# Performance work log

Measured on AMD Instinct MI355X. Metric: run time of the kernel, lower is better.

The kernel has to match this reference:

```python
import jax, jax.numpy as jnp
import numpy as np


def setup_inputs() -> dict:
    key = jax.random.key(0)
    kq, kk, kv = jax.random.split(key, 3)
    B, HQ, HKV, S, D = 1, 32, 8, 2048, 128
    return {
        "query": jax.random.normal(kq, (B, HQ, S, D), dtype=jnp.float32),
        "key": jax.random.normal(kk, (B, HKV, S, D), dtype=jnp.float32),
        "value": jax.random.normal(kv, (B, HKV, S, D), dtype=jnp.float32),
    }


def reference(query, key, value):
    # RawSDP.forward with is_causal=True, attn_mask=None, dropout_p=0, scale=None
    b, hq, sq, d = query.shape
    hkv = key.shape[1]
    reps = hq // hkv  # GQA group size
    # repeak_kv: expand each kv head `reps` times contiguously along head axis
    key = jnp.repeat(key, reps, axis=1)    # [b, hq, skv, d]
    value = jnp.repeat(value, reps, axis=1)
    skv = key.shape[2]
    half_sqrt = 1.0 / jnp.sqrt(jnp.sqrt(jnp.float32(d)))  # scale split across q and k
    scores = jnp.einsum("bhqd,bhkd->bhqk", query * half_sqrt, key * half_sqrt)
    # causal tril bool mask -> additive mask (0 where allowed, finfo.min where not)
    causal = jnp.tril(jnp.ones((sq, skv), dtype=bool))
    neg = jnp.finfo(query.dtype).min
    scores = scores + jnp.where(causal, jnp.zeros((), query.dtype), neg)
    # softmax computed in float32, cast back to query dtype
    attn = jax.nn.softmax(scores.astype(jnp.float32), axis=-1).astype(query.dtype)
    return jnp.einsum("bhqk,bhkd->bhqd", attn, value)
```

## Files before the change

kernel.cpp:

```cpp
#include <hip/hip_runtime.h>
#include <hip/hip_bf16.h>
#include <stdint.h>

typedef __attribute__((ext_vector_type(8))) short bf16x8;
typedef __attribute__((ext_vector_type(4))) float f32x4;
typedef __attribute__((ext_vector_type(16))) float f32x16;

#define S_LEN 2048
#define D_DIM 128
#define HQ_N  32
#define NT32  64
#define SUB_B 8192

__device__ __forceinline__ ushort f2bf(float f) {
  union { float f; uint32_t u; } c; c.f = f;
  uint32_t u = c.u;
  u += 0x7FFFu + ((u >> 16) & 1u);
  return (ushort)(u >> 16);
}

__device__ __forceinline__ uint32_t cvtpk(float lo, float hi) {
  uint32_t r;
  asm("v_cvt_pk_bf16_f32 %0, %1, %2" : "=v"(r) : "v"(lo), "v"(hi));
  return r;
}

__device__ __forceinline__ float xhalf_max(float x) {
  uint32_t a = __builtin_bit_cast(uint32_t, x), b;
  asm volatile("v_mov_b32 %0, %1" : "=&v"(b) : "v"(a));
  asm volatile("v_permlane32_swap_b32 %0, %1" : "+v"(a), "+v"(b));
  return fmaxf(__builtin_bit_cast(float, a), __builtin_bit_cast(float, b));
}

__global__ __launch_bounds__(256) void prep_k(const float* __restrict__ K,
                                              ushort* __restrict__ KT) {
  int tid  = blockIdx.x * 256 + threadIdx.x;
  int tile = tid >> 9;
  int c    = tid & 511;
  int s    = c >> 6;
  int lane = c & 63;
  int l31  = lane & 31, hi = lane >> 5;
  const float* src = K + ((size_t)(tile * 32 + l31)) * D_DIM + 16 * s + 8 * hi;
  float4 x = *(const float4*)src;
  float4 y = *(const float4*)(src + 4);
  union { ushort u[8]; bf16x8 v; } o;
  o.u[0] = f2bf(x.x); o.u[1] = f2bf(x.y); o.u[2] = f2bf(x.z); o.u[3] = f2bf(x.w);
  o.u[4] = f2bf(y.x); o.u[5] = f2bf(y.y); o.u[6] = f2bf(y.z); o.u[7] = f2bf(y.w);
  *(bf16x8*)(KT + (size_t)tid * 8) = o.v;
}

__global__ __launch_bounds__(256) void prep_v(const float* __restrict__ V,
                                              ushort* __restrict__ VT) {
  int tid  = blockIdx.x * 256 + threadIdx.x;
  int tile = tid >> 9;
  int cc   = tid & 511;
  int l31  = cc & 31;
  int hi   = (cc >> 5) & 1;
  int c    = (cc >> 6) & 1;
  int dt   = cc >> 7;
  int hkv  = tile >> 6, ktv = tile & 63;
  const float* src = V + ((size_t)hkv * S_LEN + ktv * 32 + 16 * c + 8 * hi) * D_DIM
                       + 32 * dt + l31;
  union { ushort u[8]; bf16x8 v; } o;
  #pragma unroll
  for (int jj = 0; jj < 8; ++jj) o.u[jj] = f2bf(src[(size_t)jj * D_DIM]);
  *(bf16x8*)(VT + (size_t)tid * 8) = o.v;
}

__global__ __launch_bounds__(256, 2) void attn_fwd(
    const float* __restrict__ Q, const ushort* __restrict__ KT,
    const ushort* __restrict__ VT, float* __restrict__ O) {
  const int id   = blockIdx.x;
  const int g    = id & 7;
  const int c    = (id >> 3) & 31;
  const int p    = (id >> 8) & 1;
  const int j    = p ? (63 - c) : c;
  const int qh   = threadIdx.x >> 6;
  const int h    = g * 4 + qh;
  const int lane = threadIdx.x & 63;
  const int l31  = lane & 31;
  const int hi   = lane >> 5;
  const int qrow = j * 32 + l31;
  const int jt   = j >> 1;

  const char* kt_base = (const char*)KT + (size_t)g * NT32 * SUB_B;
  const char* vt_base = (const char*)VT + (size_t)g * NT32 * SUB_B;

  const float scale = 0.08838834764831845f * 1.4426950408889634f;
  bf16x8 qf[8];
  {
    const float* qp = Q + ((size_t)h * S_LEN + qrow) * D_DIM;
    #pragma unroll
    for (int s = 0; s < 8; ++s) {
      const float* px = qp + 16 * s + 8 * hi;
      float4 x = *(const float4*)px;
      float4 y = *(const float4*)(px + 4);
      bf16x8 f;
      f[0] = (short)f2bf(x.x * scale); f[1] = (short)f2bf(x.y * scale);
      f[2] = (short)f2bf(x.z * scale); f[3] = (short)f2bf(x.w * scale);
      f[4] = (short)f2bf(y.x * scale); f[5] = (short)f2bf(y.y * scale);
      f[6] = (short)f2bf(y.z * scale); f[7] = (short)f2bf(y.w * scale);
      qf[s] = f;
    }
  }

  bf16x8 ones;
  #pragma unroll
  for (int s = 0; s < 8; ++s) ones[s] = (short)0x3F80;
  const f32x16 zero16 = {};

  f32x16 o4[4] = {};
  float mrow = -1e30f, lsum = 0.f;

  for (int kt = 0; kt <= jt; ++kt) {
    const char* kp = kt_base + (size_t)kt * (2 * SUB_B);

    bf16x8 kf[16];
    #pragma unroll
    for (int t = 0; t < 2; ++t)
      #pragma unroll
      for (int s = 0; s < 8; ++s)
        kf[t * 8 + s] = *(const bf16x8*)(kp + t * SUB_B + (s * 64 + lane) * 16);
    bf16x8 vfA[8], vfB[8];
    const char* vp = vt_base + (size_t)(2 * kt) * SUB_B;
    #pragma unroll
    for (int ks = 0; ks < 2; ++ks)
      #pragma unroll
      for (int dt = 0; dt < 4; ++dt)
        vfA[ks * 4 + dt] = *(const bf16x8*)(vp + (dt * 128 + ks * 64 + lane) * 16);

    f32x16 st[2] = {};
    __builtin_amdgcn_s_setprio(1);
    #pragma unroll
    for (int t = 0; t < 2; ++t)
      #pragma unroll
      for (int s = 0; s < 8; ++s)
        st[t] = __builtin_amdgcn_mfma_f32_32x32x16_bf16(kf[t * 8 + s], qf[s], st[t], 0, 0, 0);
    __builtin_amdgcn_s_setprio(0);

    #pragma unroll
    for (int ks = 0; ks < 2; ++ks)
      #pragma unroll
      for (int dt = 0; dt < 4; ++dt)
        vfB[ks * 4 + dt] = *(const bf16x8*)(vp + SUB_B + (dt * 128 + ks * 64 + lane) * 16);

    if (kt == jt) {
      #pragma unroll
      for (int t = 0; t < 2; ++t)
        #pragma unroll
        for (int r = 0; r < 16; ++r) {
          int kv = 64 * kt + 32 * t + (r & 3) + 8 * (r >> 2) + 4 * hi;
          if (kv > qrow) st[t][r] = -1e30f;
        }
    }

    float t16[8];
    #pragma unroll
    for (int e = 0; e < 8; ++e)
      t16[e] = fmaxf(fmaxf(st[0][e], st[0][e + 8]), fmaxf(st[1][e], st[1][e + 8]));
    float mx = fmaxf(fmaxf(fmaxf(t16[0], t16[1]), fmaxf(t16[2], t16[3])),
                     fmaxf(fmaxf(t16[4], t16[5]), fmaxf(t16[6], t16[7])));
    mx = xhalf_max(mx);
    if (!__all(mx <= mrow + 8.0f)) {
      float mnew = fmaxf(mrow, mx);
      float alpha = exp2f(mrow - mnew);
      #pragma unroll
      for (int dt = 0; dt < 4; ++dt) o4[dt] *= alpha;
      lsum *= alpha;
      mrow = mnew;
    }
    #pragma unroll
    for (int t = 0; t < 2; ++t)
      #pragma unroll
      for (int e = 0; e < 16; ++e) st[t][e] = exp2f(st[t][e] - mrow);

    bf16x8 pb[4];
    #pragma unroll
    for (int t = 0; t < 2; ++t)
      #pragma unroll
      for (int cc = 0; cc < 2; ++cc) {
        const int r0 = cc * 8;
        uint32_t a0 = cvtpk(st[t][r0 + 0], st[t][r0 + 1]);
        uint32_t b0 = cvtpk(st[t][r0 + 4], st[t][r0 + 5]);
        asm volatile("v_permlane32_swap_b32 %0, %1" : "+v"(a0), "+v"(b0));
        uint32_t a1 = cvtpk(st[t][r0 + 2], st[t][r0 + 3]);
        uint32_t b1 = cvtpk(st[t][r0 + 6], st[t][r0 + 7]);
        asm volatile("v_permlane32_swap_b32 %0, %1" : "+v"(a1), "+v"(b1));
        union { uint32_t u[4]; bf16x8 v; } pu;
        pu.u[0] = a0; pu.u[1] = a1; pu.u[2] = b0; pu.u[3] = b1;
        pb[t * 2 + cc] = pu.v;
      }

    f32x16 pbsum = __builtin_amdgcn_mfma_f32_32x32x16_bf16(ones, pb[0], zero16, 0, 0, 0);
    pbsum = __builtin_amdgcn_mfma_f32_32x32x16_bf16(ones, pb[1], pbsum, 0, 0, 0);
    pbsum = __builtin_amdgcn_mfma_f32_32x32x16_bf16(ones, pb[2], pbsum, 0, 0, 0);
    pbsum = __builtin_amdgcn_mfma_f32_32x32x16_bf16(ones, pb[3], pbsum, 0, 0, 0);

    __builtin_amdgcn_s_setprio(1);
    #pragma unroll
    for (int dt = 0; dt < 4; ++dt) {
      o4[dt] = __builtin_amdgcn_mfma_f32_32x32x16_bf16(vfA[0 * 4 + dt], pb[0], o4[dt], 0, 0, 0);
      o4[dt] = __builtin_amdgcn_mfma_f32_32x32x16_bf16(vfA[1 * 4 + dt], pb[1], o4[dt], 0, 0, 0);
      o4[dt] = __builtin_amdgcn_mfma_f32_32x32x16_bf16(vfB[0 * 4 + dt], pb[2], o4[dt], 0, 0, 0);
      o4[dt] = __builtin_amdgcn_mfma_f32_32x32x16_bf16(vfB[1 * 4 + dt], pb[3], o4[dt], 0, 0, 0);
    }
    __builtin_amdgcn_s_setprio(0);

    lsum += pbsum[0];

    __syncthreads();
  }

  const float inv = 1.0f / lsum;
  float* op = O + ((size_t)h * S_LEN + qrow) * D_DIM;
  #pragma unroll
  for (int dt = 0; dt < 4; ++dt)
    #pragma unroll
    for (int rq = 0; rq < 4; ++rq) {
      f32x4 vv;
      #pragma unroll
      for (int jj = 0; jj < 4; ++jj) vv[jj] = o4[dt][rq * 4 + jj] * inv;
      *(f32x4*)(op + 32 * dt + 8 * rq + 4 * hi) = vv;
    }
}

extern "C" void kernel_launch(void* const* d_in, const int* in_sizes, int n_in,
                              void* d_out, int out_size, void* d_ws, size_t ws_size,
                              hipStream_t stream) {
  const float* Q = (const float*)d_in[0];
  const float* K = (const float*)d_in[1];
  const float* V = (const float*)d_in[2];
  float* O = (float*)d_out;
  ushort* wsK = (ushort*)d_ws;
  ushort* wsV = wsK + (size_t)8 * NT32 * (SUB_B / 2);
  prep_k<<<1024, 256, 0, stream>>>(K, wsK);
  prep_v<<<1024, 256, 0, stream>>>(V, wsV);
  attn_fwd<<<512, 256, 0, stream>>>(Q, wsK, wsV, O);
}
```

Baseline: 84.88 us.

## Share K/V tiles across waves via double-buffered LDS with async global-to-LDS loads

```diff
diff --git a/kernel.cpp b/kernel.cpp
--- a/kernel.cpp
+++ b/kernel.cpp
@@ -11,6 +11,7 @@
 #define HQ_N  32
 #define NT32  64
 #define SUB_B 8192
+#define TILE_B 16384
 
 __device__ __forceinline__ ushort f2bf(float f) {
   union { float f; uint32_t u; } c; c.f = f;
@@ -30,6 +31,12 @@
   asm volatile("v_mov_b32 %0, %1" : "=&v"(b) : "v"(a));
   asm volatile("v_permlane32_swap_b32 %0, %1" : "+v"(a), "+v"(b));
   return fmaxf(__builtin_bit_cast(float, a), __builtin_bit_cast(float, b));
+}
+
+__device__ __forceinline__ void gload16(const void* g, void* l) {
+  __builtin_amdgcn_global_load_lds(
+      (const __attribute__((address_space(1))) uint32_t*)g,
+      (__attribute__((address_space(3))) uint32_t*)l, 16, 0, 0);
 }
 
 __global__ __launch_bounds__(256) void prep_k(const float* __restrict__ K,
@@ -74,17 +81,29 @@
   const int g    = id & 7;
   const int c    = (id >> 3) & 31;
   const int p    = (id >> 8) & 1;
-  const int j    = p ? (63 - c) : c;
-  const int qh   = threadIdx.x >> 6;
-  const int h    = g * 4 + qh;
+  const int qt   = p ? (15 - (c >> 2)) : (c >> 2);
+  const int h    = g * 4 + (c & 3);
+  const int w    = threadIdx.x >> 6;
   const int lane = threadIdx.x & 63;
   const int l31  = lane & 31;
   const int hi   = lane >> 5;
-  const int qrow = j * 32 + l31;
-  const int jt   = j >> 1;
+  const int qw   = qt * 128 + w * 32;
+  const int qrow = qw + l31;
+  const int ntiles = 2 * qt + 2;
+
+  __shared__ ushort Klds[2][TILE_B / 2];
+  __shared__ ushort Vlds[2][TILE_B / 2];
 
   const char* kt_base = (const char*)KT + (size_t)g * NT32 * SUB_B;
   const char* vt_base = (const char*)VT + (size_t)g * NT32 * SUB_B;
+  const int tid = threadIdx.x;
+
+  #pragma unroll
+  for (int i = 0; i < 4; ++i) {
+    int off = (tid + i * 256) * 16;
+    gload16(kt_base + off, (char*)Klds[0] + off);
+    gload16(vt_base + off, (char*)Vlds[0] + off);
+  }
 
   const float scale = 0.08838834764831845f * 1.4426950408889634f;
   bf16x8 qf[8];
@@ -112,102 +131,118 @@
   f32x16 o4[4] = {};
   float mrow = -1e30f, lsum = 0.f;
 
-  for (int kt = 0; kt <= jt; ++kt) {
-    const char* kp = kt_base + (size_t)kt * (2 * SUB_B);
-
-    bf16x8 kf[16];
-    #pragma unroll
-    for (int t = 0; t < 2; ++t)
-      #pragma unroll
-      for (int s = 0; s < 8; ++s)
-        kf[t * 8 + s] = *(const bf16x8*)(kp + t * SUB_B + (s * 64 + lane) * 16);
-    bf16x8 vfA[8], vfB[8];
-    const char* vp = vt_base + (size_t)(2 * kt) * SUB_B;
-    #pragma unroll
-    for (int ks = 0; ks < 2; ++ks)
-      #pragma unroll
-      for (int dt = 0; dt < 4; ++dt)
-        vfA[ks * 4 + dt] = *(const bf16x8*)(vp + (dt * 128 + ks * 64 + lane) * 16);
-
-    f32x16 st[2] = {};
-    __builtin_amdgcn_s_setprio(1);
-    #pragma unroll
-    for (int t = 0; t < 2; ++t)
-      #pragma unroll
-      for (int s = 0; s < 8; ++s)
-        st[t] = __builtin_amdgcn_mfma_f32_32x32x16_bf16(kf[t * 8 + s], qf[s], st[t], 0, 0, 0);
-    __builtin_amdgcn_s_setprio(0);
-
-    #pragma unroll
-    for (int ks = 0; ks < 2; ++ks)
-      #pragma unroll
-      for (int dt = 0; dt < 4; ++dt)
-        vfB[ks * 4 + dt] = *(const bf16x8*)(vp + SUB_B + (dt * 128 + ks * 64 + lane) * 16);
-
-    if (kt == jt) {
-      #pragma unroll
-      for (int t = 0; t < 2; ++t)
-        #pragma unroll
-        for (int r = 0; r < 16; ++r) {
-          int kv = 64 * kt + 32 * t + (r & 3) + 8 * (r >> 2) + 4 * hi;
-          if (kv > qrow) st[t][r] = -1e30f;
+  __syncthreads();
+
+  for (int kt = 0; kt < ntiles; ++kt) {
+    const int cur = kt & 1;
+
+    if (kt + 1 < ntiles) {
+      const char* gk = kt_base + (size_t)(kt + 1) * TILE_B;
+      const char* gv = vt_base + (size_t)(kt + 1) * TILE_B;
+      #pragma unroll
+      for (int i = 0; i < 4; ++i) {
+        int off = (tid + i * 256) * 16;
+        gload16(gk + off, (char*)Klds[cur ^ 1] + off);
+        gload16(gv + off, (char*)Vlds[cur ^ 1] + off);
+      }
+    }
+
+    if (64 * kt <= qw + 31) {
+      const char* kp = (const char*)Klds[cur];
+      const char* vp = (const char*)Vlds[cur];
+
+      bf16x8 kf[16];
+      #pragma unroll
+      for (int t = 0; t < 2; ++t)
+        #pragma unroll
+        for (int s = 0; s < 8; ++s)
+          kf[t * 8 + s] = *(const bf16x8*)(kp + t * SUB_B + (s * 64 + lane) * 16);
+      bf16x8 vfA[8], vfB[8];
+      #pragma unroll
+      for (int ks = 0; ks < 2; ++ks)
+        #pragma unroll
+        for (int dt = 0; dt < 4; ++dt)
+          vfA[ks * 4 + dt] = *(const bf16x8*)(vp + (dt * 128 + ks * 64 + lane) * 16);
+
+      f32x16 st[2] = {};
+      __builtin_amdgcn_s_setprio(1);
+      #pragma unroll
+      for (int t = 0; t < 2; ++t)
+        #pragma unroll
+        for (int s = 0; s < 8; ++s)
+          st[t] = __builtin_amdgcn_mfma_f32_32x32x16_bf16(kf[t * 8 + s], qf[s], st[t], 0, 0, 0);
+      __builtin_amdgcn_s_setprio(0);
+
+      #pragma unroll
+      for (int ks = 0; ks < 2; ++ks)
+        #pragma unroll
+        for (int dt = 0; dt < 4; ++dt)
+          vfB[ks * 4 + dt] = *(const bf16x8*)(vp + SUB_B + (dt * 128 + ks * 64 + lane) * 16);
+
+      if (64 * kt + 63 > qw) {
+        #pragma unroll
+        for (int t = 0; t < 2; ++t)
+          #pragma unroll
+          for (int r = 0; r < 16; ++r) {
+            int kv = 64 * kt + 32 * t + (r & 3) + 8 * (r >> 2) + 4 * hi;
+            if (kv > qrow) st[t][r] = -1e30f;
+          }
+      }
+
+      float t16[8];
+      #pragma unroll
+      for (int e = 0; e < 8; ++e)
+        t16[e] = fmaxf(fmaxf(st[0][e], st[0][e + 8]), fmaxf(st[1][e], st[1][e + 8]));
+      float mx = fmaxf(fmaxf(fmaxf(t16[0], t16[1]), fmaxf(t16[2], t16[3])),
+                       fmaxf(fmaxf(t16[4], t16[5]), fmaxf(t16[6], t16[7])));
+      mx = xhalf_max(mx);
+      if (!__all(mx <= mrow + 8.0f)) {
+        float mnew = fmaxf(mrow, mx);
+        float alpha = exp2f(mrow - mnew);
+        #pragma unroll
+        for (int dt = 0; dt < 4; ++dt) o4[dt] *= alpha;
+        lsum *= alpha;
+        mrow = mnew;
+      }
+      #pragma unroll
+      for (int t = 0; t < 2; ++t)
+        #pragma unroll
+        for (int e = 0; e < 16; ++e) st[t][e] = exp2f(st[t][e] - mrow);
+
+      bf16x8 pb[4];
+      #pragma unroll
+      for (int t = 0; t < 2; ++t)
+        #pragma unroll
+        for (int cc = 0; cc < 2; ++cc) {
+          const int r0 = cc * 8;
+          uint32_t a0 = cvtpk(st[t][r0 + 0], st[t][r0 + 1]);
+          uint32_t b0 = cvtpk(st[t][r0 + 4], st[t][r0 + 5]);
+          asm volatile("v_permlane32_swap_b32 %0, %1" : "+v"(a0), "+v"(b0));
+          uint32_t a1 = cvtpk(st[t][r0 + 2], st[t][r0 + 3]);
+          uint32_t b1 = cvtpk(st[t][r0 + 6], st[t][r0 + 7]);
+          asm volatile("v_permlane32_swap_b32 %0, %1" : "+v"(a1), "+v"(b1));
+          union { uint32_t u[4]; bf16x8 v; } pu;
+          pu.u[0] = a0; pu.u[1] = a1; pu.u[2] = b0; pu.u[3] = b1;
+          pb[t * 2 + cc] = pu.v;
         }
-    }
-
-    float t16[8];
-    #pragma unroll
-    for (int e = 0; e < 8; ++e)
-      t16[e] = fmaxf(fmaxf(st[0][e], st[0][e + 8]), fmaxf(st[1][e], st[1][e + 8]));
-    float mx = fmaxf(fmaxf(fmaxf(t16[0], t16[1]), fmaxf(t16[2], t16[3])),
-                     fmaxf(fmaxf(t16[4], t16[5]), fmaxf(t16[6], t16[7])));
-    mx = xhalf_max(mx);
-    if (!__all(mx <= mrow + 8.0f)) {
-      float mnew = fmaxf(mrow, mx);
-      float alpha = exp2f(mrow - mnew);
-      #pragma unroll
-      for (int dt = 0; dt < 4; ++dt) o4[dt] *= alpha;
-      lsum *= alpha;
-      mrow = mnew;
-    }
-    #pragma unroll
-    for (int t = 0; t < 2; ++t)
-      #pragma unroll
-      for (int e = 0; e < 16; ++e) st[t][e] = exp2f(st[t][e] - mrow);
-
-    bf16x8 pb[4];
-    #pragma unroll
-    for (int t = 0; t < 2; ++t)
-      #pragma unroll
-      for (int cc = 0; cc < 2; ++cc) {
-        const int r0 = cc * 8;
-        uint32_t a0 = cvtpk(st[t][r0 + 0], st[t][r0 + 1]);
-        uint32_t b0 = cvtpk(st[t][r0 + 4], st[t][r0 + 5]);
-        asm volatile("v_permlane32_swap_b32 %0, %1" : "+v"(a0), "+v"(b0));
-        uint32_t a1 = cvtpk(st[t][r0 + 2], st[t][r0 + 3]);
-        uint32_t b1 = cvtpk(st[t][r0 + 6], st[t][r0 + 7]);
-        asm volatile("v_permlane32_swap_b32 %0, %1" : "+v"(a1), "+v"(b1));
-        union { uint32_t u[4]; bf16x8 v; } pu;
-        pu.u[0] = a0; pu.u[1] = a1; pu.u[2] = b0; pu.u[3] = b1;
-        pb[t * 2 + cc] = pu.v;
-      }
-
-    f32x16 pbsum = __builtin_amdgcn_mfma_f32_32x32x16_bf16(ones, pb[0], zero16, 0, 0, 0);
-    pbsum = __builtin_amdgcn_mfma_f32_32x32x16_bf16(ones, pb[1], pbsum, 0, 0, 0);
-    pbsum = __builtin_amdgcn_mfma_f32_32x32x16_bf16(ones, pb[2], pbsum, 0, 0, 0);
-    pbsum = __builtin_amdgcn_mfma_f32_32x32x16_bf16(ones, pb[3], pbsum, 0, 0, 0);
-
-    __builtin_amdgcn_s_setprio(1);
-    #pragma unroll
-    for (int dt = 0; dt < 4; ++dt) {
-      o4[dt] = __builtin_amdgcn_mfma_f32_32x32x16_bf16(vfA[0 * 4 + dt], pb[0], o4[dt], 0, 0, 0);
-      o4[dt] = __builtin_amdgcn_mfma_f32_32x32x16_bf16(vfA[1 * 4 + dt], pb[1], o4[dt], 0, 0, 0);
-      o4[dt] = __builtin_amdgcn_mfma_f32_32x32x16_bf16(vfB[0 * 4 + dt], pb[2], o4[dt], 0, 0, 0);
-      o4[dt] = __builtin_amdgcn_mfma_f32_32x32x16_bf16(vfB[1 * 4 + dt], pb[3], o4[dt], 0, 0, 0);
-    }
-    __builtin_amdgcn_s_setprio(0);
-
-    lsum += pbsum[0];
-
+
+      f32x16 pbsum = __builtin_amdgcn_mfma_f32_32x32x16_bf16(ones, pb[0], zero16, 0, 0, 0);
+      pbsum = __builtin_amdgcn_mfma_f32_32x32x16_bf16(ones, pb[1], pbsum, 0, 0, 0);
+      pbsum = __builtin_amdgcn_mfma_f32_32x32x16_bf16(ones, pb[2], pbsum, 0, 0, 0);
+      pbsum = __builtin_amdgcn_mfma_f32_32x32x16_bf16(ones, pb[3], pbsum, 0, 0, 0);
+
+      __builtin_amdgcn_s_setprio(1);
+      #pragma unroll
+      for (int dt = 0; dt < 4; ++dt) {
+        o4[dt] = __builtin_amdgcn_mfma_f32_32x32x16_bf16(vfA[0 * 4 + dt], pb[0], o4[dt], 0, 0, 0);
+        o4[dt] = __builtin_amdgcn_mfma_f32_32x32x16_bf16(vfA[1 * 4 + dt], pb[1], o4[dt], 0, 0, 0);
+        o4[dt] = __builtin_amdgcn_mfma_f32_32x32x16_bf16(vfB[0 * 4 + dt], pb[2], o4[dt], 0, 0, 0);
+        o4[dt] = __builtin_amdgcn_mfma_f32_32x32x16_bf16(vfB[1 * 4 + dt], pb[3], o4[dt], 0, 0, 0);
+      }
+      __builtin_amdgcn_s_setprio(0);
+
+      lsum += pbsum[0];
+    }
     __syncthreads();
   }
 
```

Result: no change. 86.15 us (+1.5%).
